# Optimization experiments

Hardware: AMD Instinct MI355X
Metric: run time of the kernel (lower is better)

## Reference

```python
import jax, jax.numpy as jnp
import numpy as np

N_SRC = 16384
N_NBR = 16384
E = 524288
D = 128
ALPHA = 0.2  # leaky_relu slope


def setup_inputs() -> dict:
    key = jax.random.key(0)
    ks = jax.random.split(key, 16)
    s = lambda k, shape, fan: jax.random.normal(k, shape, jnp.float32) / np.sqrt(fan)
    x_cur = jax.random.normal(ks[0], (N_SRC, D), jnp.float32)
    x_nbr = jax.random.normal(ks[1], (N_NBR, D), jnp.float32)
    W1c = s(ks[2], (D, D), D); b1c = jnp.zeros((D,), jnp.float32)
    W2c = s(ks[3], (D, D), D); b2c = jnp.zeros((D,), jnp.float32)
    W1n = s(ks[4], (D, D), D); b1n = jnp.zeros((D,), jnp.float32)
    W2n = s(ks[5], (D, D), D); b2n = jnp.zeros((D,), jnp.float32)
    Wa = s(ks[6], (2 * D, 1), 2 * D); ba = jnp.zeros((1,), jnp.float32)
    src = jax.random.randint(ks[7], (E,), 0, N_SRC, jnp.int32)
    dst = jax.random.randint(ks[8], (E,), 0, N_NBR, jnp.int32)
    edges = jnp.stack([src, dst], axis=1)  # [E, 2]
    return dict(x_cur=x_cur, x_nbr=x_nbr, W1c=W1c, b1c=b1c, W2c=W2c, b2c=b2c,
                W1n=W1n, b1n=b1n, W2n=W2n, b2n=b2n, Wa=Wa, ba=ba, edges=edges)


def reference(x_cur, x_nbr, W1c, b1c, W2c, b2c, W1n, b1n, W2n, b2n, Wa, ba, edges):
    src, dst = edges[:, 0], edges[:, 1]
    # hidden MLPs (keras Dense with default activation=None -> linear stack)
    cur = (x_cur @ W1c + b1c) @ W2c + b2c          # [N_src, D]
    nbr = (x_nbr @ W1n + b1n) @ W2n + b2n          # [N_nbr, D]
    # per-edge gather + concat + attention MLP
    pair = jnp.concatenate([cur[src], nbr[dst]], axis=1)   # [E, 2D]
    scores = jax.nn.leaky_relu((pair @ Wa + ba)[:, 0], ALPHA)  # [E]
    # segment softmax over source node
    exp_s = jnp.exp(scores)
    seg_sum = jax.ops.segment_sum(exp_s, src, num_segments=N_SRC)  # [N_src]
    norm_s = exp_s / seg_sum[src]                                   # [E]
    # scatter to dense adjacency and matmul (faithful to tf.scatter_nd + matmul)
    adj = jnp.zeros((N_SRC, N_NBR), jnp.float32).at[src, dst].add(norm_s)
    return adj @ nbr                                # [N_src, D]
```

## Files before the change

### kernel.cpp

```cpp
#include <hip/hip_runtime.h>
#include <hip/hip_bf16.h>

#define NSRC 16384
#define NNBR 16384
#define NE   524288
#define DDIM 128
#define ALPHA_C 0.2f
#define CAP 128

#define SCAT_BLKS (NE / 512)
#define GEMM_BLKS (NNBR / 32)
#define ACUR_BLKS (NSRC / 8)

typedef __hip_bfloat16 bf16;

__device__ __forceinline__ float b2f(bf16 v) { return __bfloat162float(v); }
__device__ __forceinline__ float us2f(unsigned short u) {
    return __uint_as_float(((unsigned)u) << 16);
}
__device__ __forceinline__ unsigned short f2us(float f) {
    bf16 h = __float2bfloat16(f);
    return *reinterpret_cast<unsigned short*>(&h);
}
__device__ __forceinline__ float LD(const void* p, int i, bool f32) {
    return f32 ? ((const float*)p)[i] : b2f(((const bf16*)p)[i]);
}
__device__ __forceinline__ bool detect_f32(const unsigned short* xprobe, int t, int* s_flag) {
    if (t < 64) {
        int ex = (xprobe[2 * t] >> 7) & 0xFF;
        unsigned long long m = __ballot(ex >= 0xC0);
        if (t == 0) *s_flag = (__popcll(m) >= 2) ? 1 : 0;
    }
    __syncthreads();
    return *s_flag != 0;
}

__global__ __launch_bounds__(1024) void k_prep(const unsigned short* __restrict__ xprobe,
                             const void* __restrict__ W1c, const void* __restrict__ b1c,
                             const void* __restrict__ W2c, const void* __restrict__ b2c,
                             const void* __restrict__ W1n, const void* __restrict__ b1n,
                             const void* __restrict__ W2n, const void* __restrict__ b2n,
                             const void* __restrict__ Wa, const void* __restrict__ ba,
                             int* __restrict__ flagp, float* __restrict__ u_c,
                             float* __restrict__ wan, float* __restrict__ bn,
                             float* __restrict__ c0, float* __restrict__ baf,
                             float* __restrict__ M, int* __restrict__ cursor) {
    __shared__ int s_flag;
    __shared__ float tc[DDIM], wa_s[DDIM];
    __shared__ float sred[2];
    __shared__ float w1r[8][DDIM];
    int t = threadIdx.x;

    if (blockIdx.x == 17) {
#pragma unroll
        for (int i = 0; i < NSRC / 1024; i++) cursor[i * 1024 + t] = 0;
        return;
    }
    const bool f32 = detect_f32(xprobe, t, &s_flag);

    if (blockIdx.x != 0) {
        int i0 = (blockIdx.x - 1) * 8;
        int r = t >> 7, j = t & 127;
        w1r[r][j] = LD(W1n, (i0 + r) * DDIM + j, f32);
        __syncthreads();
        float s = 0.f;
        if (f32) {
            const float* p = (const float*)W2n + j;
#pragma unroll 8
            for (int k = 0; k < DDIM; k++) s += w1r[r][k] * p[k * DDIM];
        } else {
            const bf16* p = (const bf16*)W2n + j;
#pragma unroll 8
            for (int k = 0; k < DDIM; k++) s += w1r[r][k] * b2f(p[k * DDIM]);
        }
        M[(i0 + r) * DDIM + j] = s;
        return;
    }

    if (t == 0) { flagp[0] = f32 ? 1 : 0; baf[0] = LD(ba, 0, f32); }
    if (t < DDIM) wa_s[t] = LD(Wa, t, f32);
    else if (t < 2 * DDIM) wan[t - DDIM] = LD(Wa, t, f32);
    __syncthreads();

    int row = t >> 3, sub = t & 7, k0 = sub * 16;
    float s = 0.f, bb = 0.f;
    if (f32) {
        const float* w2c = (const float*)W2c + row * DDIM + k0;
        const float* b1nf = (const float*)b1n;
        const float* w2n = (const float*)W2n;
#pragma unroll
        for (int k = 0; k < 16; k++) {
            s  += w2c[k] * wa_s[k0 + k];
            bb += b1nf[k0 + k] * w2n[(k0 + k) * DDIM + row];
        }
    } else {
        const bf16* w2c = (const bf16*)W2c + row * DDIM + k0;
        const bf16* b1nh = (const bf16*)b1n;
        const bf16* w2n = (const bf16*)W2n;
#pragma unroll
        for (int k = 0; k < 16; k++) {
            s  += b2f(w2c[k]) * wa_s[k0 + k];
            bb += b2f(b1nh[k0 + k]) * b2f(w2n[(k0 + k) * DDIM + row]);
        }
    }
    s  += __shfl_xor(s, 1, 64);  s  += __shfl_xor(s, 2, 64);  s  += __shfl_xor(s, 4, 64);
    bb += __shfl_xor(bb, 1, 64); bb += __shfl_xor(bb, 2, 64); bb += __shfl_xor(bb, 4, 64);
    if (sub == 0) { tc[row] = s; bn[row] = bb + LD(b2n, row, f32); }
    __syncthreads();

    float u = 0.f;
    if (f32) {
        const float* w1c = (const float*)W1c + row * DDIM + k0;
#pragma unroll
        for (int k = 0; k < 16; k++) u += w1c[k] * tc[k0 + k];
    } else {
        const bf16* w1c = (const bf16*)W1c + row * DDIM + k0;
#pragma unroll
        for (int k = 0; k < 16; k++) u += b2f(w1c[k]) * tc[k0 + k];
    }
    u += __shfl_xor(u, 1, 64); u += __shfl_xor(u, 2, 64); u += __shfl_xor(u, 4, 64);
    if (sub == 0) u_c[row] = u;

    if (t < 128) {
        float v = LD(b1c, t, f32) * tc[t] + LD(b2c, t, f32) * wa_s[t];
#pragma unroll
        for (int o = 32; o > 0; o >>= 1) v += __shfl_down(v, o, 64);
        if ((t & 63) == 0) sred[t >> 6] = v;
    }
    __syncthreads();
    if (t == 0) c0[0] = sred[0] + sred[1];
}

__global__ __launch_bounds__(128) void k_main(const void* __restrict__ Xn,
                                              const void* __restrict__ Xc,
                                              const float* __restrict__ M,
                                              const float* __restrict__ bn,
                                              const float* __restrict__ wan,
                                              const float* __restrict__ u_c,
                                              const float* __restrict__ c0,
                                              const int* __restrict__ flagp,
                                              const int2* __restrict__ edges2,
                                              int* __restrict__ cursor,
                                              unsigned short* __restrict__ bucket,
                                              unsigned short* __restrict__ Y,
                                              float* __restrict__ a_nbr,
                                              float* __restrict__ a_cur) {
    int t = threadIdx.x;
    int b = blockIdx.x;

    if (b < SCAT_BLKS) {
        int4 p0 = reinterpret_cast<const int4*>(edges2)[t + b * 256];
        int4 p1 = reinterpret_cast<const int4*>(edges2)[t + b * 256 + 128];
        int p;
        p = atomicAdd(cursor + p0.x, 1);
        if (p < CAP) bucket[p0.x * CAP + p] = (unsigned short)p0.y;
        p = atomicAdd(cursor + p0.z, 1);
        if (p < CAP) bucket[p0.z * CAP + p] = (unsigned short)p0.w;
        p = atomicAdd(cursor + p1.x, 1);
        if (p < CAP) bucket[p1.x * CAP + p] = (unsigned short)p1.y;
        p = atomicAdd(cursor + p1.z, 1);
        if (p < CAP) bucket[p1.z * CAP + p] = (unsigned short)p1.w;
        return;
    }

    bool f32 = flagp[0] != 0;
    if (b >= SCAT_BLKS + GEMM_BLKS) {
        int base = (b - SCAT_BLKS - GEMM_BLKS) * 8 + (t >> 6) * 4;
        int lane = t & 63;
        float cc = c0[0];
        float w0 = u_c[2 * lane], w1 = u_c[2 * lane + 1];
#pragma unroll
        for (int it = 0; it < 4; it++) {
            int gw = base + it;
            float v0, v1;
            if (f32) {
                float2 v = reinterpret_cast<const float2*>((const float*)Xc + (size_t)gw * DDIM)[lane];
                v0 = v.x; v1 = v.y;
            } else {
                unsigned v = reinterpret_cast<const unsigned*>((const unsigned short*)Xc + (size_t)gw * DDIM)[lane];
                v0 = us2f((unsigned short)(v & 0xffffu));
                v1 = us2f((unsigned short)(v >> 16));
            }
            float acc = v0 * w0 + v1 * w1;
#pragma unroll
            for (int o = 32; o > 0; o >>= 1) acc += __shfl_down(acc, o, 64);
            if (lane == 0) a_cur[gw] = acc + cc;
        }
        return;
    }

    __shared__ unsigned short xs[32][DDIM];
    int rg = t >> 5, cg = t & 31;
    int row0 = (b - SCAT_BLKS) * 32;
    if (f32) {
        const float4* px = reinterpret_cast<const float4*>((const float*)Xn + (size_t)row0 * DDIM);
#pragma unroll
        for (int q = 0; q < 8; q++) {
            int idx = q * 128 + t;
            float4 v = px[idx];
            int rr = idx >> 5, c = (idx & 31) * 4;
            ushort4 y; y.x = f2us(v.x); y.y = f2us(v.y); y.z = f2us(v.z); y.w = f2us(v.w);
            *reinterpret_cast<ushort4*>(&xs[rr][c]) = y;
        }
    } else {
        const ushort4* px = reinterpret_cast<const ushort4*>((const bf16*)Xn + (size_t)row0 * DDIM);
#pragma unroll
        for (int q = 0; q < 8; q++) {
            int idx = q * 128 + t;
            int rr = idx >> 5, c = (idx & 31) * 4;
            *reinterpret_cast<ushort4*>(&xs[rr][c]) = px[idx];
        }
    }
    __syncthreads();
    float acc[8][4];
    float4 bb = reinterpret_cast<const float4*>(bn)[cg];
#pragma unroll
    for (int rr = 0; rr < 8; rr++) {
        acc[rr][0] = bb.x; acc[rr][1] = bb.y; acc[rr][2] = bb.z; acc[rr][3] = bb.w;
    }
    const float4* Mp = reinterpret_cast<const float4*>(M) + cg;
#pragma unroll 2
    for (int k0 = 0; k0 < DDIM; k0 += 4) {
        float4 m0 = Mp[(k0 + 0) * 32];
        float4 m1 = Mp[(k0 + 1) * 32];
        float4 m2 = Mp[(k0 + 2) * 32];
        float4 m3 = Mp[(k0 + 3) * 32];
#pragma unroll
        for (int rr = 0; rr < 8; rr++) {
            ushort4 xk = *reinterpret_cast<const ushort4*>(&xs[rg * 8 + rr][k0]);
            float x0 = us2f(xk.x), x1 = us2f(xk.y), x2 = us2f(xk.z), x3 = us2f(xk.w);
            acc[rr][0] += x0 * m0.x + x1 * m1.x + x2 * m2.x + x3 * m3.x;
            acc[rr][1] += x0 * m0.y + x1 * m1.y + x2 * m2.y + x3 * m3.y;
            acc[rr][2] += x0 * m0.z + x1 * m1.z + x2 * m2.z + x3 * m3.z;
            acc[rr][3] += x0 * m0.w + x1 * m1.w + x2 * m2.w + x3 * m3.w;
        }
    }
    float4 wn = reinterpret_cast<const float4*>(wan)[cg];
#pragma unroll
    for (int rr = 0; rr < 8; rr++) {
        int row = row0 + rg * 8 + rr;
        ushort4 y;
        y.x = f2us(acc[rr][0]); y.y = f2us(acc[rr][1]);
        y.z = f2us(acc[rr][2]); y.w = f2us(acc[rr][3]);
        reinterpret_cast<ushort4*>(Y + (size_t)row * DDIM)[cg] = y;
        float v = acc[rr][0] * wn.x + acc[rr][1] * wn.y + acc[rr][2] * wn.z + acc[rr][3] * wn.w;
        v += __shfl_xor(v, 1, 64); v += __shfl_xor(v, 2, 64); v += __shfl_xor(v, 4, 64);
        v += __shfl_xor(v, 8, 64); v += __shfl_xor(v, 16, 64);
        if (cg == 0) a_nbr[row] = v;
    }
}

__global__ __launch_bounds__(256) void k_aggregate(const int* __restrict__ cursor,
                                                   const unsigned short* __restrict__ bucket,
                                                   const float* __restrict__ a_cur,
                                                   const float* __restrict__ a_nbr,
                                                   const float* __restrict__ baf,
                                                   const unsigned short* __restrict__ nbr,
                                                   float* __restrict__ out) {
    int gw = blockIdx.x * 4 + (threadIdx.x >> 6);
    int lane = threadIdx.x & 63;
    int g = lane >> 3;
    int sub = lane & 7;
    int cnt = cursor[gw];
    cnt = cnt < CAP ? cnt : CAP;
    const unsigned short* bp = bucket + (size_t)gw * CAP;
    float acb = a_cur[gw] + baf[0];
    const uint4 z4 = make_uint4(0, 0, 0, 0);
    float acc[16];
#pragma unroll
    for (int k = 0; k < 16; k++) acc[k] = 0.f;
    float den = 0.f;

#define LOADE(J, Dv, ANv, V0v, V1v)                                                  \
    do {                                                                             \
        int j_ = (J); bool a_ = j_ < cnt;                                            \
        Dv = a_ ? (int)bp[j_] : 0;                                                   \
        ANv = a_ ? a_nbr[Dv] : -1e30f;                                               \
        if (a_) {                                                                    \
            const uint4* p_ = reinterpret_cast<const uint4*>(nbr + (size_t)Dv * DDIM + sub * 16); \
            V0v = p_[0]; V1v = p_[1];                                                \
        } else { V0v = z4; V1v = z4; }                                               \
    } while (0)

#define CONSUME(ANv, V0v, V1v)                                                       \
    do {                                                                             \
        float sc_ = acb + ANv;                                                       \
        sc_ = sc_ > 0.f ? sc_ : ALPHA_C * sc_;                                       \
        sc_ = fminf(sc_, 80.f);                                                      \
        float w_ = __expf(sc_);                                                      \
        den += w_;                                                                   \
        acc[0]  += w_ * us2f((unsigned short)(V0v.x & 0xffffu));                     \
        acc[1]  += w_ * us2f((unsigned short)(V0v.x >> 16));                         \
        acc[2]  += w_ * us2f((unsigned short)(V0v.y & 0xffffu));                     \
        acc[3]  += w_ * us2f((unsigned short)(V0v.y >> 16));                         \
        acc[4]  += w_ * us2f((unsigned short)(V0v.z & 0xffffu));                     \
        acc[5]  += w_ * us2f((unsigned short)(V0v.z >> 16));                         \
        acc[6]  += w_ * us2f((unsigned short)(V0v.w & 0xffffu));                     \
        acc[7]  += w_ * us2f((unsigned short)(V0v.w >> 16));                         \
        acc[8]  += w_ * us2f((unsigned short)(V1v.x & 0xffffu));                     \
        acc[9]  += w_ * us2f((unsigned short)(V1v.x >> 16));                         \
        acc[10] += w_ * us2f((unsigned short)(V1v.y & 0xffffu));                     \
        acc[11] += w_ * us2f((unsigned short)(V1v.y >> 16));                         \
        acc[12] += w_ * us2f((unsigned short)(V1v.z & 0xffffu));                     \
        acc[13] += w_ * us2f((unsigned short)(V1v.z >> 16));                         \
        acc[14] += w_ * us2f((unsigned short)(V1v.w & 0xffffu));                     \
        acc[15] += w_ * us2f((unsigned short)(V1v.w >> 16));                         \
    } while (0)

    if (cnt > 0) {
        int dA; float anA; uint4 vA0, vA1;
        int dB; float anB; uint4 vB0, vB1;
        LOADE(g, dA, anA, vA0, vA1);
        LOADE(8 + g, dB, anB, vB0, vB1);
        for (int base = 0; base < cnt; base += 16) {
            CONSUME(anA, vA0, vA1);
            LOADE(base + 16 + g, dA, anA, vA0, vA1);
            CONSUME(anB, vB0, vB1);
            LOADE(base + 24 + g, dB, anB, vB0, vB1);
        }
    }
#undef LOADE
#undef CONSUME

#pragma unroll
    for (int k = 0; k < 16; k++) {
        acc[k] += __shfl_xor(acc[k], 8, 64);
        acc[k] += __shfl_xor(acc[k], 16, 64);
        acc[k] += __shfl_xor(acc[k], 32, 64);
    }
    den += __shfl_xor(den, 8, 64);
    den += __shfl_xor(den, 16, 64);
    den += __shfl_xor(den, 32, 64);
    float inv = den > 0.f ? 1.f / den : 0.f;
    if (g == 0) {
        float4* po = reinterpret_cast<float4*>(out + (size_t)gw * DDIM + sub * 16);
        po[0] = make_float4(acc[0] * inv, acc[1] * inv, acc[2] * inv, acc[3] * inv);
        po[1] = make_float4(acc[4] * inv, acc[5] * inv, acc[6] * inv, acc[7] * inv);
        po[2] = make_float4(acc[8] * inv, acc[9] * inv, acc[10] * inv, acc[11] * inv);
        po[3] = make_float4(acc[12] * inv, acc[13] * inv, acc[14] * inv, acc[15] * inv);
    }
}

extern "C" void kernel_launch(void* const* d_in, const int* in_sizes, int n_in,
                              void* d_out, int out_size, void* d_ws, size_t ws_size,
                              hipStream_t stream) {
    const void* x_cur = d_in[0];
    const void* x_nbr = d_in[1];
    const void* W1c = d_in[2];
    const void* b1c = d_in[3];
    const void* W2c = d_in[4];
    const void* b2c = d_in[5];
    const void* W1n = d_in[6];
    const void* b1n = d_in[7];
    const void* W2n = d_in[8];
    const void* b2n = d_in[9];
    const void* Wa  = d_in[10];
    const void* ba  = d_in[11];
    const int2* edges2 = (const int2*)d_in[12];
    float* out = (float*)d_out;

    char* w = (char*)d_ws;
    size_t off = 0;
    auto alloc = [&](size_t b) { size_t o = off; off = (off + b + 255) & ~(size_t)255; return o; };
    float* M      = (float*)(w + alloc(DDIM * DDIM * 4));
    float* u_c    = (float*)(w + alloc(DDIM * 4));
    float* wan    = (float*)(w + alloc(DDIM * 4));
    float* bn     = (float*)(w + alloc(DDIM * 4));
    float* c0     = (float*)(w + alloc(4));
    float* baf    = (float*)(w + alloc(4));
    int*   flag   = (int*)(w + alloc(4));
    float* a_cur  = (float*)(w + alloc(NSRC * 4));
    float* a_nbr  = (float*)(w + alloc(NNBR * 4));
    int* cursor   = (int*)(w + alloc(NSRC * 4));
    unsigned short* bucket = (unsigned short*)(w + alloc((size_t)NSRC * CAP * 2));
    unsigned short* nbr = (unsigned short*)(w + alloc((size_t)NNBR * DDIM * 2));

    k_prep<<<18, 1024, 0, stream>>>((const unsigned short*)x_cur, W1c, b1c, W2c, b2c,
                                    W1n, b1n, W2n, b2n, Wa, ba, flag, u_c, wan, bn, c0, baf,
                                    M, cursor);
    k_main<<<SCAT_BLKS + GEMM_BLKS + ACUR_BLKS, 128, 0, stream>>>(
        x_nbr, x_cur, M, bn, wan, u_c, c0, flag, edges2, cursor, bucket, nbr, a_nbr, a_cur);
    k_aggregate<<<NSRC / 4, 256, 0, stream>>>(cursor, bucket, a_cur, a_nbr, baf, nbr, out);
}
```

Measured before the change: 165.8 us.

## Fuse three kernels into one cooperative persistent kernel with grid syncs

Merges the prep, main (scatter/GEMM/a_cur) and aggregate kernels into a single cooperative kernel. Blocks loop over work units in a grid-stride pattern, and phases are separated by grid-wide syncs. This removes two kernel launches and their boundaries, at the cost of grid-sync overhead and a capped grid of at most 1024 blocks of 256 threads. Work granularity also changes: the GEMM uses 256-thread blocks computing 4 rows per thread group, and prep splits the M computation into 64 units.

```diff
diff --git a/kernel.cpp b/kernel.cpp
--- a/kernel.cpp
+++ b/kernel.cpp
@@ -1,5 +1,8 @@
 #include <hip/hip_runtime.h>
 #include <hip/hip_bf16.h>
+#include <hip/hip_cooperative_groups.h>
+
+namespace cg = cooperative_groups;
 
 #define NSRC 16384
 #define NNBR 16384
@@ -8,9 +11,10 @@
 #define ALPHA_C 0.2f
 #define CAP 128
 
-#define SCAT_BLKS (NE / 512)
-#define GEMM_BLKS (NNBR / 32)
-#define ACUR_BLKS (NSRC / 8)
+#define SCAT_U 512
+#define GEMM_U 512
+#define ACUR_U 1024
+#define AGG_U  4096
 
 typedef __hip_bfloat16 bf16;
 
@@ -35,249 +39,234 @@
     return *s_flag != 0;
 }
 
-__global__ __launch_bounds__(1024) void k_prep(const unsigned short* __restrict__ xprobe,
-                             const void* __restrict__ W1c, const void* __restrict__ b1c,
-                             const void* __restrict__ W2c, const void* __restrict__ b2c,
-                             const void* __restrict__ W1n, const void* __restrict__ b1n,
-                             const void* __restrict__ W2n, const void* __restrict__ b2n,
-                             const void* __restrict__ Wa, const void* __restrict__ ba,
-                             int* __restrict__ flagp, float* __restrict__ u_c,
-                             float* __restrict__ wan, float* __restrict__ bn,
-                             float* __restrict__ c0, float* __restrict__ baf,
-                             float* __restrict__ M, int* __restrict__ cursor) {
+struct KParams {
+    const unsigned short* xprobe;
+    const void* Xn; const void* Xc;
+    const void* W1c; const void* b1c; const void* W2c; const void* b2c;
+    const void* W1n; const void* b1n; const void* W2n; const void* b2n;
+    const void* Wa;  const void* ba;
+    const int2* edges2;
+    float* u_c; float* wan; float* bn; float* c0; float* baf; float* M;
+    int* cursor;
+    unsigned short* bucket;
+    unsigned short* Y;
+    float* a_nbr; float* a_cur;
+    float* out;
+};
+
+__global__ __launch_bounds__(256, 4) void k_all(KParams p) {
+    __shared__ __align__(16) char smem[8192];
     __shared__ int s_flag;
-    __shared__ float tc[DDIM], wa_s[DDIM];
     __shared__ float sred[2];
-    __shared__ float w1r[8][DDIM];
-    int t = threadIdx.x;
-
-    if (blockIdx.x == 17) {
-#pragma unroll
-        for (int i = 0; i < NSRC / 1024; i++) cursor[i * 1024 + t] = 0;
-        return;
+    cg::grid_group gg = cg::this_grid();
+    const int t = threadIdx.x;
+    const int b = blockIdx.x;
+    const int GD = gridDim.x;
+
+    const bool f32 = detect_f32(p.xprobe, t, &s_flag);
+
+    for (int i = b * 256 + t; i < NSRC; i += GD * 256) p.cursor[i] = 0;
+
+    float* tc   = (float*)smem;
+    float* wa_s = tc + DDIM;
+    for (int u = b; u < 1 + 64; u += GD) {
+        __syncthreads();
+        if (u == 0) {
+            if (t < DDIM) wa_s[t] = LD(p.Wa, t, f32);
+            else p.wan[t - DDIM] = LD(p.Wa, t, f32);
+            __syncthreads();
+            int row = t >> 1, sub = t & 1, k0 = sub * 64;
+            float s = 0.f, bb = 0.f;
+            if (f32) {
+                const float* w2c = (const float*)p.W2c + row * DDIM + k0;
+                const float* b1nf = (const float*)p.b1n;
+                const float* w2n = (const float*)p.W2n;
+#pragma unroll 8
+                for (int k = 0; k < 64; k++) {
+                    s  += w2c[k] * wa_s[k0 + k];
+                    bb += b1nf[k0 + k] * w2n[(k0 + k) * DDIM + row];
+                }
+            } else {
+                const bf16* w2c = (const bf16*)p.W2c + row * DDIM + k0;
+                const bf16* b1nh = (const bf16*)p.b1n;
+                const bf16* w2n = (const bf16*)p.W2n;
+#pragma unroll 8
+                for (int k = 0; k < 64; k++) {
+                    s  += b2f(w2c[k]) * wa_s[k0 + k];
+                    bb += b2f(b1nh[k0 + k]) * b2f(w2n[(k0 + k) * DDIM + row]);
+                }
+            }
+            s  += __shfl_xor(s, 1, 64);
+            bb += __shfl_xor(bb, 1, 64);
+            if (sub == 0) { tc[row] = s; p.bn[row] = bb + LD(p.b2n, row, f32); }
+            __syncthreads();
+            float uu = 0.f;
+            if (f32) {
+                const float* w1c = (const float*)p.W1c + row * DDIM + k0;
+#pragma unroll 8
+                for (int k = 0; k < 64; k++) uu += w1c[k] * tc[k0 + k];
+            } else {
+                const bf16* w1c = (const bf16*)p.W1c + row * DDIM + k0;
+#pragma unroll 8
+                for (int k = 0; k < 64; k++) uu += b2f(w1c[k]) * tc[k0 + k];
+            }
+            uu += __shfl_xor(uu, 1, 64);
+            if (sub == 0) p.u_c[row] = uu;
+            if (t < DDIM) {
+                float v = LD(p.b1c, t, f32) * tc[t] + LD(p.b2c, t, f32) * wa_s[t];
+#pragma unroll
+                for (int o = 32; o > 0; o >>= 1) v += __shfl_down(v, o, 64);
+                if ((t & 63) == 0) sred[t >> 6] = v;
+            }
+            __syncthreads();
+            if (t == 0) { p.c0[0] = sred[0] + sred[1]; p.baf[0] = LD(p.ba, 0, f32); }
+        } else {
+            float* w1r = (float*)smem;
+            int i0 = (u - 1) * 2;
+            int r = t >> 7, j = t & 127;
+            w1r[r * DDIM + j] = LD(p.W1n, (i0 + r) * DDIM + j, f32);
+            __syncthreads();
+            float s = 0.f;
+            if (f32) {
+                const float* q = (const float*)p.W2n + j;
+#pragma unroll 8
+                for (int k = 0; k < DDIM; k++) s += w1r[r * DDIM + k] * q[k * DDIM];
+            } else {
+                const bf16* q = (const bf16*)p.W2n + j;
+#pragma unroll 8
+                for (int k = 0; k < DDIM; k++) s += w1r[r * DDIM + k] * b2f(q[k * DDIM]);
+            }
+            p.M[(i0 + r) * DDIM + j] = s;
+        }
     }
-    const bool f32 = detect_f32(xprobe, t, &s_flag);
-
-    if (blockIdx.x != 0) {
-        int i0 = (blockIdx.x - 1) * 8;
-        int r = t >> 7, j = t & 127;
-        w1r[r][j] = LD(W1n, (i0 + r) * DDIM + j, f32);
-        __syncthreads();
-        float s = 0.f;
-        if (f32) {
-            const float* p = (const float*)W2n + j;
-#pragma unroll 8
-            for (int k = 0; k < DDIM; k++) s += w1r[r][k] * p[k * DDIM];
+
+    gg.sync();
+
+    unsigned short (*xs)[DDIM] = reinterpret_cast<unsigned short(*)[DDIM]>(smem);
+    const int4* e4 = reinterpret_cast<const int4*>(p.edges2);
+    for (int u = b; u < SCAT_U + GEMM_U + ACUR_U; u += GD) {
+        if (u < SCAT_U) {
+            int4 p0 = e4[u * 512 + t];
+            int4 p1 = e4[u * 512 + 256 + t];
+            int q_;
+            q_ = atomicAdd(p.cursor + p0.x, 1);
+            if (q_ < CAP) p.bucket[p0.x * CAP + q_] = (unsigned short)p0.y;
+            q_ = atomicAdd(p.cursor + p0.z, 1);
+            if (q_ < CAP) p.bucket[p0.z * CAP + q_] = (unsigned short)p0.w;
+            q_ = atomicAdd(p.cursor + p1.x, 1);
+            if (q_ < CAP) p.bucket[p1.x * CAP + q_] = (unsigned short)p1.y;
+            q_ = atomicAdd(p.cursor + p1.z, 1);
+            if (q_ < CAP) p.bucket[p1.z * CAP + q_] = (unsigned short)p1.w;
+        } else if (u < SCAT_U + GEMM_U) {
+            __syncthreads();
+            int gu = u - SCAT_U;
+            int rg = t >> 5, cg2 = t & 31;
+            int row0 = gu * 32;
+            if (f32) {
+                const float4* px = reinterpret_cast<const float4*>((const float*)p.Xn + (size_t)row0 * DDIM);
+#pragma unroll
+                for (int q = 0; q < 4; q++) {
+                    int idx = q * 256 + t;
+                    float4 v = px[idx];
+                    int rr = idx >> 5, c = (idx & 31) * 4;
+                    ushort4 y; y.x = f2us(v.x); y.y = f2us(v.y); y.z = f2us(v.z); y.w = f2us(v.w);
+                    *reinterpret_cast<ushort4*>(&xs[rr][c]) = y;
+                }
+            } else {
+                const ushort4* px = reinterpret_cast<const ushort4*>((const bf16*)p.Xn + (size_t)row0 * DDIM);
+#pragma unroll
+                for (int q = 0; q < 4; q++) {
+                    int idx = q * 256 + t;
+                    int rr = idx >> 5, c = (idx & 31) * 4;
+                    *reinterpret_cast<ushort4*>(&xs[rr][c]) = px[idx];
+                }
+            }
+            __syncthreads();
+            float acc[4][4];
+            float4 bb4 = reinterpret_cast<const float4*>(p.bn)[cg2];
+#pragma unroll
+            for (int rr = 0; rr < 4; rr++) {
+                acc[rr][0] = bb4.x; acc[rr][1] = bb4.y; acc[rr][2] = bb4.z; acc[rr][3] = bb4.w;
+            }
+            const float4* Mp = reinterpret_cast<const float4*>(p.M) + cg2;
+#pragma unroll 2
+            for (int k0 = 0; k0 < DDIM; k0 += 4) {
+                float4 m0 = Mp[(k0 + 0) * 32];
+                float4 m1 = Mp[(k0 + 1) * 32];
+                float4 m2 = Mp[(k0 + 2) * 32];
+                float4 m3 = Mp[(k0 + 3) * 32];
+#pragma unroll
+                for (int rr = 0; rr < 4; rr++) {
+                    ushort4 xk = *reinterpret_cast<const ushort4*>(&xs[rg * 4 + rr][k0]);
+                    float x0 = us2f(xk.x), x1 = us2f(xk.y), x2 = us2f(xk.z), x3 = us2f(xk.w);
+                    acc[rr][0] += x0 * m0.x + x1 * m1.x + x2 * m2.x + x3 * m3.x;
+                    acc[rr][1] += x0 * m0.y + x1 * m1.y + x2 * m2.y + x3 * m3.y;
+                    acc[rr][2] += x0 * m0.z + x1 * m1.z + x2 * m2.z + x3 * m3.z;
+                    acc[rr][3] += x0 * m0.w + x1 * m1.w + x2 * m2.w + x3 * m3.w;
+                }
+            }
+            float4 wn = reinterpret_cast<const float4*>(p.wan)[cg2];
+#pragma unroll
+            for (int rr = 0; rr < 4; rr++) {
+                int row = row0 + rg * 4 + rr;
+                ushort4 y;
+                y.x = f2us(acc[rr][0]); y.y = f2us(acc[rr][1]);
+                y.z = f2us(acc[rr][2]); y.w = f2us(acc[rr][3]);
+                reinterpret_cast<ushort4*>(p.Y + (size_t)row * DDIM)[cg2] = y;
+                float v = acc[rr][0] * wn.x + acc[rr][1] * wn.y + acc[rr][2] * wn.z + acc[rr][3] * wn.w;
+                v += __shfl_xor(v, 1, 64); v += __shfl_xor(v, 2, 64); v += __shfl_xor(v, 4, 64);
+                v += __shfl_xor(v, 8, 64); v += __shfl_xor(v, 16, 64);
+                if (cg2 == 0) p.a_nbr[row] = v;
+            }
         } else {
-            const bf16* p = (const bf16*)W2n + j;
-#pragma unroll 8
-            for (int k = 0; k < DDIM; k++) s += w1r[r][k] * b2f(p[k * DDIM]);
-        }
-        M[(i0 + r) * DDIM + j] = s;
-        return;
+            int base = (u - SCAT_U - GEMM_U) * 16 + (t >> 6) * 4;
+            int lane = t & 63;
+            float cc = p.c0[0];
+            float w0 = p.u_c[2 * lane], w1 = p.u_c[2 * lane + 1];
+#pragma unroll
+            for (int it = 0; it < 4; it++) {
+                int gw = base + it;
+                float v0, v1;
+                if (f32) {
+                    float2 v = reinterpret_cast<const float2*>((const float*)p.Xc + (size_t)gw * DDIM)[lane];
+                    v0 = v.x; v1 = v.y;
+                } else {
+                    unsigned v = reinterpret_cast<const unsigned*>((const unsigned short*)p.Xc + (size_t)gw * DDIM)[lane];
+                    v0 = us2f((unsigned short)(v & 0xffffu));
+                    v1 = us2f((unsigned short)(v >> 16));
+                }
+                float a = v0 * w0 + v1 * w1;
+#pragma unroll
+                for (int o = 32; o > 0; o >>= 1) a += __shfl_down(a, o, 64);
+                if (lane == 0) p.a_cur[gw] = a + cc;
+            }
+        }
     }
 
-    if (t == 0) { flagp[0] = f32 ? 1 : 0; baf[0] = LD(ba, 0, f32); }
-    if (t < DDIM) wa_s[t] = LD(Wa, t, f32);
-    else if (t < 2 * DDIM) wan[t - DDIM] = LD(Wa, t, f32);
-    __syncthreads();
-
-    int row = t >> 3, sub = t & 7, k0 = sub * 16;
-    float s = 0.f, bb = 0.f;
-    if (f32) {
-        const float* w2c = (const float*)W2c + row * DDIM + k0;
-        const float* b1nf = (const float*)b1n;
-        const float* w2n = (const float*)W2n;
-#pragma unroll
-        for (int k = 0; k < 16; k++) {
-            s  += w2c[k] * wa_s[k0 + k];
-            bb += b1nf[k0 + k] * w2n[(k0 + k) * DDIM + row];
-        }
-    } else {
-        const bf16* w2c = (const bf16*)W2c + row * DDIM + k0;
-        const bf16* b1nh = (const bf16*)b1n;
-        const bf16* w2n = (const bf16*)W2n;
-#pragma unroll
-        for (int k = 0; k < 16; k++) {
-            s  += b2f(w2c[k]) * wa_s[k0 + k];
-            bb += b2f(b1nh[k0 + k]) * b2f(w2n[(k0 + k) * DDIM + row]);
-        }
-    }
-    s  += __shfl_xor(s, 1, 64);  s  += __shfl_xor(s, 2, 64);  s  += __shfl_xor(s, 4, 64);
-    bb += __shfl_xor(bb, 1, 64); bb += __shfl_xor(bb, 2, 64); bb += __shfl_xor(bb, 4, 64);
-    if (sub == 0) { tc[row] = s; bn[row] = bb + LD(b2n, row, f32); }
-    __syncthreads();
-
-    float u = 0.f;
-    if (f32) {
-        const float* w1c = (const float*)W1c + row * DDIM + k0;
-#pragma unroll
-        for (int k = 0; k < 16; k++) u += w1c[k] * tc[k0 + k];
-    } else {
-        const bf16* w1c = (const bf16*)W1c + row * DDIM + k0;
-#pragma unroll
-        for (int k = 0; k < 16; k++) u += b2f(w1c[k]) * tc[k0 + k];
-    }
-    u += __shfl_xor(u, 1, 64); u += __shfl_xor(u, 2, 64); u += __shfl_xor(u, 4, 64);
-    if (sub == 0) u_c[row] = u;
-
-    if (t < 128) {
-        float v = LD(b1c, t, f32) * tc[t] + LD(b2c, t, f32) * wa_s[t];
-#pragma unroll
-        for (int o = 32; o > 0; o >>= 1) v += __shfl_down(v, o, 64);
-        if ((t & 63) == 0) sred[t >> 6] = v;
-    }
-    __syncthreads();
-    if (t == 0) c0[0] = sred[0] + sred[1];
-}
-
-__global__ __launch_bounds__(128) void k_main(const void* __restrict__ Xn,
-                                              const void* __restrict__ Xc,
-                                              const float* __restrict__ M,
-                                              const float* __restrict__ bn,
-                                              const float* __restrict__ wan,
-                                              const float* __restrict__ u_c,
-                                              const float* __restrict__ c0,
-                                              const int* __restrict__ flagp,
-                                              const int2* __restrict__ edges2,
-                                              int* __restrict__ cursor,
-                                              unsigned short* __restrict__ bucket,
-                                              unsigned short* __restrict__ Y,
-                                              float* __restrict__ a_nbr,
-                                              float* __restrict__ a_cur) {
-    int t = threadIdx.x;
-    int b = blockIdx.x;
-
-    if (b < SCAT_BLKS) {
-        int4 p0 = reinterpret_cast<const int4*>(edges2)[t + b * 256];
-        int4 p1 = reinterpret_cast<const int4*>(edges2)[t + b * 256 + 128];
-        int p;
-        p = atomicAdd(cursor + p0.x, 1);
-        if (p < CAP) bucket[p0.x * CAP + p] = (unsigned short)p0.y;
-        p = atomicAdd(cursor + p0.z, 1);
-        if (p < CAP) bucket[p0.z * CAP + p] = (unsigned short)p0.w;
-        p = atomicAdd(cursor + p1.x, 1);
-        if (p < CAP) bucket[p1.x * CAP + p] = (unsigned short)p1.y;
-        p = atomicAdd(cursor + p1.z, 1);
-        if (p < CAP) bucket[p1.z * CAP + p] = (unsigned short)p1.w;
-        return;
-    }
-
-    bool f32 = flagp[0] != 0;
-    if (b >= SCAT_BLKS + GEMM_BLKS) {
-        int base = (b - SCAT_BLKS - GEMM_BLKS) * 8 + (t >> 6) * 4;
+    gg.sync();
+
+    for (int u = b; u < AGG_U; u += GD) {
+        int gw = u * 4 + (t >> 6);
         int lane = t & 63;
-        float cc = c0[0];
-        float w0 = u_c[2 * lane], w1 = u_c[2 * lane + 1];
-#pragma unroll
-        for (int it = 0; it < 4; it++) {
-            int gw = base + it;
-            float v0, v1;
-            if (f32) {
-                float2 v = reinterpret_cast<const float2*>((const float*)Xc + (size_t)gw * DDIM)[lane];
-                v0 = v.x; v1 = v.y;
-            } else {
-                unsigned v = reinterpret_cast<const unsigned*>((const unsigned short*)Xc + (size_t)gw * DDIM)[lane];
-                v0 = us2f((unsigned short)(v & 0xffffu));
-                v1 = us2f((unsigned short)(v >> 16));
-            }
-            float acc = v0 * w0 + v1 * w1;
-#pragma unroll
-            for (int o = 32; o > 0; o >>= 1) acc += __shfl_down(acc, o, 64);
-            if (lane == 0) a_cur[gw] = acc + cc;
-        }
-        return;
-    }
-
-    __shared__ unsigned short xs[32][DDIM];
-    int rg = t >> 5, cg = t & 31;
-    int row0 = (b - SCAT_BLKS) * 32;
-    if (f32) {
-        const float4* px = reinterpret_cast<const float4*>((const float*)Xn + (size_t)row0 * DDIM);
-#pragma unroll
-        for (int q = 0; q < 8; q++) {
-            int idx = q * 128 + t;
-            float4 v = px[idx];
-            int rr = idx >> 5, c = (idx & 31) * 4;
-            ushort4 y; y.x = f2us(v.x); y.y = f2us(v.y); y.z = f2us(v.z); y.w = f2us(v.w);
-            *reinterpret_cast<ushort4*>(&xs[rr][c]) = y;
-        }
-    } else {
-        const ushort4* px = reinterpret_cast<const ushort4*>((const bf16*)Xn + (size_t)row0 * DDIM);
-#pragma unroll
-        for (int q = 0; q < 8; q++) {
-            int idx = q * 128 + t;
-            int rr = idx >> 5, c = (idx & 31) * 4;
-            *reinterpret_cast<ushort4*>(&xs[rr][c]) = px[idx];
-        }
-    }
-    __syncthreads();
-    float acc[8][4];
-    float4 bb = reinterpret_cast<const float4*>(bn)[cg];
-#pragma unroll
-    for (int rr = 0; rr < 8; rr++) {
-        acc[rr][0] = bb.x; acc[rr][1] = bb.y; acc[rr][2] = bb.z; acc[rr][3] = bb.w;
-    }
-    const float4* Mp = reinterpret_cast<const float4*>(M) + cg;
-#pragma unroll 2
-    for (int k0 = 0; k0 < DDIM; k0 += 4) {
-        float4 m0 = Mp[(k0 + 0) * 32];
-        float4 m1 = Mp[(k0 + 1) * 32];
-        float4 m2 = Mp[(k0 + 2) * 32];
-        float4 m3 = Mp[(k0 + 3) * 32];
-#pragma unroll
-        for (int rr = 0; rr < 8; rr++) {
-            ushort4 xk = *reinterpret_cast<const ushort4*>(&xs[rg * 8 + rr][k0]);
-            float x0 = us2f(xk.x), x1 = us2f(xk.y), x2 = us2f(xk.z), x3 = us2f(xk.w);
-            acc[rr][0] += x0 * m0.x + x1 * m1.x + x2 * m2.x + x3 * m3.x;
-            acc[rr][1] += x0 * m0.y + x1 * m1.y + x2 * m2.y + x3 * m3.y;
-            acc[rr][2] += x0 * m0.z + x1 * m1.z + x2 * m2.z + x3 * m3.z;
-            acc[rr][3] += x0 * m0.w + x1 * m1.w + x2 * m2.w + x3 * m3.w;
-        }
-    }
-    float4 wn = reinterpret_cast<const float4*>(wan)[cg];
-#pragma unroll
-    for (int rr = 0; rr < 8; rr++) {
-        int row = row0 + rg * 8 + rr;
-        ushort4 y;
-        y.x = f2us(acc[rr][0]); y.y = f2us(acc[rr][1]);
-        y.z = f2us(acc[rr][2]); y.w = f2us(acc[rr][3]);
-        reinterpret_cast<ushort4*>(Y + (size_t)row * DDIM)[cg] = y;
-        float v = acc[rr][0] * wn.x + acc[rr][1] * wn.y + acc[rr][2] * wn.z + acc[rr][3] * wn.w;
-        v += __shfl_xor(v, 1, 64); v += __shfl_xor(v, 2, 64); v += __shfl_xor(v, 4, 64);
-        v += __shfl_xor(v, 8, 64); v += __shfl_xor(v, 16, 64);
-        if (cg == 0) a_nbr[row] = v;
-    }
-}
-
-__global__ __launch_bounds__(256) void k_aggregate(const int* __restrict__ cursor,
-                                                   const unsigned short* __restrict__ bucket,
-                                                   const float* __restrict__ a_cur,
-                                                   const float* __restrict__ a_nbr,
-                                                   const float* __restrict__ baf,
-                                                   const unsigned short* __restrict__ nbr,
-                                                   float* __restrict__ out) {
-    int gw = blockIdx.x * 4 + (threadIdx.x >> 6);
-    int lane = threadIdx.x & 63;
-    int g = lane >> 3;
-    int sub = lane & 7;
-    int cnt = cursor[gw];
-    cnt = cnt < CAP ? cnt : CAP;
-    const unsigned short* bp = bucket + (size_t)gw * CAP;
-    float acb = a_cur[gw] + baf[0];
-    const uint4 z4 = make_uint4(0, 0, 0, 0);
-    float acc[16];
-#pragma unroll
-    for (int k = 0; k < 16; k++) acc[k] = 0.f;
-    float den = 0.f;
+        int g = lane >> 3;
+        int sub = lane & 7;
+        int cnt = p.cursor[gw];
+        cnt = cnt < CAP ? cnt : CAP;
+        const unsigned short* bp = p.bucket + (size_t)gw * CAP;
+        float acb = p.a_cur[gw] + p.baf[0];
+        const uint4 z4 = make_uint4(0, 0, 0, 0);
+        float acc[16];
+#pragma unroll
+        for (int k = 0; k < 16; k++) acc[k] = 0.f;
+        float den = 0.f;
 
 #define LOADE(J, Dv, ANv, V0v, V1v)                                                  \
     do {                                                                             \
         int j_ = (J); bool a_ = j_ < cnt;                                            \
         Dv = a_ ? (int)bp[j_] : 0;                                                   \
-        ANv = a_ ? a_nbr[Dv] : -1e30f;                                               \
+        ANv = a_ ? p.a_nbr[Dv] : -1e30f;                                             \
         if (a_) {                                                                    \
-            const uint4* p_ = reinterpret_cast<const uint4*>(nbr + (size_t)Dv * DDIM + sub * 16); \
+            const uint4* p_ = reinterpret_cast<const uint4*>(p.Y + (size_t)Dv * DDIM + sub * 16); \
             V0v = p_[0]; V1v = p_[1];                                                \
         } else { V0v = z4; V1v = z4; }                                               \
     } while (0)
@@ -307,78 +296,77 @@
         acc[15] += w_ * us2f((unsigned short)(V1v.w >> 16));                         \
     } while (0)
 
-    if (cnt > 0) {
-        int dA; float anA; uint4 vA0, vA1;
-        int dB; float anB; uint4 vB0, vB1;
-        LOADE(g, dA, anA, vA0, vA1);
-        LOADE(8 + g, dB, anB, vB0, vB1);
-        for (int base = 0; base < cnt; base += 16) {
-            CONSUME(anA, vA0, vA1);
-            LOADE(base + 16 + g, dA, anA, vA0, vA1);
-            CONSUME(anB, vB0, vB1);
-            LOADE(base + 24 + g, dB, anB, vB0, vB1);
-        }
-    }
+        if (cnt > 0) {
+            int dA; float anA; uint4 vA0, vA1;
+            int dB; float anB; uint4 vB0, vB1;
+            LOADE(g, dA, anA, vA0, vA1);
+            LOADE(8 + g, dB, anB, vB0, vB1);
+            for (int base = 0; base < cnt; base += 16) {
+                CONSUME(anA, vA0, vA1);
+                LOADE(base + 16 + g, dA, anA, vA0, vA1);
+                CONSUME(anB, vB0, vB1);
+                LOADE(base + 24 + g, dB, anB, vB0, vB1);
+            }
+        }
 #undef LOADE
 #undef CONSUME
 
 #pragma unroll
-    for (int k = 0; k < 16; k++) {
-        acc[k] += __shfl_xor(acc[k], 8, 64);
-        acc[k] += __shfl_xor(acc[k], 16, 64);
-        acc[k] += __shfl_xor(acc[k], 32, 64);
-    }
-    den += __shfl_xor(den, 8, 64);
-    den += __shfl_xor(den, 16, 64);
-    den += __shfl_xor(den, 32, 64);
-    float inv = den > 0.f ? 1.f / den : 0.f;
-    if (g == 0) {
-        float4* po = reinterpret_cast<float4*>(out + (size_t)gw * DDIM + sub * 16);
-        po[0] = make_float4(acc[0] * inv, acc[1] * inv, acc[2] * inv, acc[3] * inv);
-        po[1] = make_float4(acc[4] * inv, acc[5] * inv, acc[6] * inv, acc[7] * inv);
-        po[2] = make_float4(acc[8] * inv, acc[9] * inv, acc[10] * inv, acc[11] * inv);
-        po[3] = make_float4(acc[12] * inv, acc[13] * inv, acc[14] * inv, acc[15] * inv);
+        for (int k = 0; k < 16; k++) {
+            acc[k] += __shfl_xor(acc[k], 8, 64);
+            acc[k] += __shfl_xor(acc[k], 16, 64);
+            acc[k] += __shfl_xor(acc[k], 32, 64);
+        }
+        den += __shfl_xor(den, 8, 64);
+        den += __shfl_xor(den, 16, 64);
+        den += __shfl_xor(den, 32, 64);
+        float inv = den > 0.f ? 1.f / den : 0.f;
+        if (g == 0) {
+            float4* po = reinterpret_cast<float4*>(p.out + (size_t)gw * DDIM + sub * 16);
+            po[0] = make_float4(acc[0] * inv, acc[1] * inv, acc[2] * inv, acc[3] * inv);
+            po[1] = make_float4(acc[4] * inv, acc[5] * inv, acc[6] * inv, acc[7] * inv);
+            po[2] = make_float4(acc[8] * inv, acc[9] * inv, acc[10] * inv, acc[11] * inv);
+            po[3] = make_float4(acc[12] * inv, acc[13] * inv, acc[14] * inv, acc[15] * inv);
+        }
     }
 }
 
 extern "C" void kernel_launch(void* const* d_in, const int* in_sizes, int n_in,
                               void* d_out, int out_size, void* d_ws, size_t ws_size,
                               hipStream_t stream) {
-    const void* x_cur = d_in[0];
-    const void* x_nbr = d_in[1];
-    const void* W1c = d_in[2];
-    const void* b1c = d_in[3];
-    const void* W2c = d_in[4];
-    const void* b2c = d_in[5];
-    const void* W1n = d_in[6];
-    const void* b1n = d_in[7];
-    const void* W2n = d_in[8];
-    const void* b2n = d_in[9];
-    const void* Wa  = d_in[10];
-    const void* ba  = d_in[11];
-    const int2* edges2 = (const int2*)d_in[12];
-    float* out = (float*)d_out;
-
     char* w = (char*)d_ws;
     size_t off = 0;
-    auto alloc = [&](size_t b) { size_t o = off; off = (off + b + 255) & ~(size_t)255; return o; };
+    auto alloc = [&](size_t bsz) { size_t o = off; off = (off + bsz + 255) & ~(size_t)255; return o; };
     float* M      = (float*)(w + alloc(DDIM * DDIM * 4));
     float* u_c    = (float*)(w + alloc(DDIM * 4));
     float* wan    = (float*)(w + alloc(DDIM * 4));
     float* bn     = (float*)(w + alloc(DDIM * 4));
     float* c0     = (float*)(w + alloc(4));
     float* baf    = (float*)(w + alloc(4));
-    int*   flag   = (int*)(w + alloc(4));
     float* a_cur  = (float*)(w + alloc(NSRC * 4));
     float* a_nbr  = (float*)(w + alloc(NNBR * 4));
     int* cursor   = (int*)(w + alloc(NSRC * 4));
     unsigned short* bucket = (unsigned short*)(w + alloc((size_t)NSRC * CAP * 2));
     unsigned short* nbr = (unsigned short*)(w + alloc((size_t)NNBR * DDIM * 2));
 
-    k_prep<<<18, 1024, 0, stream>>>((const unsigned short*)x_cur, W1c, b1c, W2c, b2c,
-                                    W1n, b1n, W2n, b2n, Wa, ba, flag, u_c, wan, bn, c0, baf,
-                                    M, cursor);
-    k_main<<<SCAT_BLKS + GEMM_BLKS + ACUR_BLKS, 128, 0, stream>>>(
-        x_nbr, x_cur, M, bn, wan, u_c, c0, flag, edges2, cursor, bucket, nbr, a_nbr, a_cur);
-    k_aggregate<<<NSRC / 4, 256, 0, stream>>>(cursor, bucket, a_cur, a_nbr, baf, nbr, out);
-}
+    KParams prm;
+    prm.xprobe = (const unsigned short*)d_in[0];
+    prm.Xn = d_in[1]; prm.Xc = d_in[0];
+    prm.W1c = d_in[2]; prm.b1c = d_in[3]; prm.W2c = d_in[4]; prm.b2c = d_in[5];
+    prm.W1n = d_in[6]; prm.b1n = d_in[7]; prm.W2n = d_in[8]; prm.b2n = d_in[9];
+    prm.Wa = d_in[10]; prm.ba = d_in[11];
+    prm.edges2 = (const int2*)d_in[12];
+    prm.u_c = u_c; prm.wan = wan; prm.bn = bn; prm.c0 = c0; prm.baf = baf; prm.M = M;
+    prm.cursor = cursor; prm.bucket = bucket; prm.Y = nbr;
+    prm.a_nbr = a_nbr; prm.a_cur = a_cur;
+    prm.out = (float*)d_out;
+
+    int maxb = 0;
+    (void)hipOccupancyMaxActiveBlocksPerMultiprocessor(&maxb, k_all, 256, 0);
+    if (maxb < 1) maxb = 1;
+    int grid = maxb * 256;
+    if (grid > 1024) grid = 1024;
+
+    void* args[] = { &prm };
+    hipLaunchCooperativeKernel((void*)k_all, dim3(grid), dim3(256), args, 0, stream);
+}
```

Measured after the change: 299.4 us. 80.6% more time.
